# Optimization experiments

Hardware: AMD Instinct MI355X
Metric: run time of the kernel (lower is better)

## Reference

```python
import jax, jax.numpy as jnp
import numpy as np

IN_F = 1024
HID_F = 4096
OUT_F = 1024
B = 64
D = 768
SPARSE_RATIO = 0.1


def setup_inputs() -> dict:
    key = jax.random.key(0)
    k_x, k_w1, k_w2, k_b, k_m = jax.random.split(key, 5)
    # x: [batch, tokens(d), in_features(s)]
    x = jax.random.normal(k_x, (B, D, IN_F), dtype=jnp.float32)
    # scale weights like typical init so GELU inputs stay in a sane range
    fc1_w = jax.random.normal(k_w1, (HID_F, IN_F), dtype=jnp.float32) * (1.0 / np.sqrt(IN_F))
    fc2_w = jax.random.normal(k_w2, (OUT_F, HID_F), dtype=jnp.float32) * (1.0 / np.sqrt(HID_F))
    fc2_b = jax.random.normal(k_b, (OUT_F,), dtype=jnp.float32) * 0.02
    sparse_mask = (jax.random.uniform(k_m, (IN_F, OUT_F)) < SPARSE_RATIO).astype(jnp.float32)
    return {"x": x, "fc1_w": fc1_w, "fc2_w": fc2_w, "fc2_b": fc2_b, "sparse_mask": sparse_mask}


def reference(x, fc1_w, fc2_w, fc2_b, sparse_mask):
    # attn_s[s,t] = sum_d fc1_w[d,s] * fc2_w[t,d] + fc2_b[t]   -> [in, out]
    attn = (jnp.einsum('ds,td->st', fc1_w, fc2_w) + fc2_b) * sparse_mask
    # dropout with p=0.0 is the identity
    out = jnp.einsum('bds,st->bdt', x, attn)  # [B, D, out]
    # torch nn.GELU default is the exact (erf) variant
    return jax.nn.gelu(out, approximate=False)
```

## Files before the change

kernel.cpp:

```cpp
#include <hip/hip_runtime.h>
#include <hip/hip_bf16.h>
#include <math.h>

typedef __attribute__((ext_vector_type(8))) short  short8;
typedef __attribute__((ext_vector_type(4))) float  floatx4;
typedef __attribute__((ext_vector_type(4))) int    i32x4;

__device__ __forceinline__ ushort f2bf(float f) {
    __hip_bfloat16 hb = __float2bfloat16(f);
    return *(ushort*)&hb;
}
__device__ __forceinline__ short8 pack8(float4 a, float4 b) {
    union { short8 v; ushort u[8]; } r;
    r.u[0] = f2bf(a.x); r.u[1] = f2bf(a.y); r.u[2] = f2bf(a.z); r.u[3] = f2bf(a.w);
    r.u[4] = f2bf(b.x); r.u[5] = f2bf(b.y); r.u[6] = f2bf(b.z); r.u[7] = f2bf(b.w);
    return r.v;
}

typedef __attribute__((address_space(1))) const void* gas1_t;
typedef __attribute__((address_space(3))) void*       las3_t;
__device__ __forceinline__ void gload16(const void* g, void* l) {
    __builtin_amdgcn_global_load_lds((gas1_t)g, (las3_t)l, 16, 0, 0);
}
__device__ __forceinline__ short8 ds_read16(uint off) {
    union { i32x4 i; short8 s; } u;
    asm volatile("ds_read_b128 %0, %1" : "=v"(u.i) : "v"(off));
    return u.s;
}

__global__ __launch_bounds__(256) void k_cvt(const float* __restrict__ in,
                                             ushort* __restrict__ out, int n8) {
    int i = blockIdx.x * 256 + threadIdx.x;
    if (i >= n8) return;
    const float4* p = reinterpret_cast<const float4*>(in) + (size_t)i * 2;
    float4 a = p[0], b = p[1];
    *reinterpret_cast<short8*>(out + (size_t)i * 8) = pack8(a, b);
}

__global__ __launch_bounds__(256) void k_transpose(const float* __restrict__ in,
                                                   ushort* __restrict__ out) {
    __shared__ float sm[64][65];
    const int tid = threadIdx.x;
    const int s0 = blockIdx.x * 64;
    const int d0 = blockIdx.y * 64;
#pragma unroll
    for (int i = 0; i < 4; ++i) {
        int lin = i * 256 + tid;
        int dr  = lin >> 4;
        int sc4 = lin & 15;
        float4 v = *reinterpret_cast<const float4*>(&in[(size_t)(d0 + dr) * 1024 + s0 + sc4 * 4]);
        sm[dr][sc4 * 4 + 0] = v.x; sm[dr][sc4 * 4 + 1] = v.y;
        sm[dr][sc4 * 4 + 2] = v.z; sm[dr][sc4 * 4 + 3] = v.w;
    }
    __syncthreads();
#pragma unroll
    for (int i = 0; i < 8; ++i) {
        int lin = i * 256 + tid;
        int dc2 = lin & 31;
        int sr  = lin >> 5;
        uint lo = (uint)f2bf(sm[dc2 * 2][sr]);
        uint hi = (uint)f2bf(sm[dc2 * 2 + 1][sr]);
        *reinterpret_cast<uint*>(&out[(size_t)(s0 + sr) * 4096 + d0 + dc2 * 2]) = lo | (hi << 16);
    }
}

template <int BM, int BN, int EPI, int SWZ>
__global__ __launch_bounds__(256) void k_gemm_b(const ushort* __restrict__ A,
                                                const ushort* __restrict__ B,
                                                const float* __restrict__ bias,
                                                const float* __restrict__ mask,
                                                void* __restrict__ Cout,
                                                int lda, int ldb, int ksteps) {
    __shared__ ushort As[BM * 32];
    __shared__ ushort Bs[BN * 32];
    const int tid  = threadIdx.x;
    const int wave = tid >> 6, lane = tid & 63;
    const int wm = wave >> 1, wn = wave & 1;
    const int quad = lane >> 4, m16 = lane & 15;

    if (EPI == 2) {
        const int sp = blockIdx.z;
        A += (size_t)sp * 1024;
        B += (size_t)sp * 1024;
        Cout = (void*)((float*)Cout + (size_t)sp * 1048576);
    }

    int bx = blockIdx.x, by = blockIdx.y;
    if (SWZ) {
        const int nx   = gridDim.x;
        const int nwg  = nx * gridDim.y;
        const int orig = by * nx + bx;
        const int cpx  = nwg >> 3;
        const int w    = (orig & 7) * cpx + (orig >> 3);
        bx = w % nx; by = w / nx;
    }
    const int n0 = bx * BN;
    const int m0 = by * BM;

    constexpr int AI = BM / 32;
    constexpr int BJ = BN / 32;
    floatx4 acc[AI][BJ];
    const floatx4 zero = {0.f, 0.f, 0.f, 0.f};
#pragma unroll
    for (int i = 0; i < AI; ++i)
#pragma unroll
        for (int j = 0; j < BJ; ++j) acc[i][j] = zero;

    const int gr = lane >> 2;
    const int gc = (lane & 3) * 8;

    for (int kt = 0; kt < ksteps; ++kt) {
        const int k0 = kt * 32;
        if (kt) __syncthreads();
#pragma unroll
        for (int t = 0; t < BM / 64; ++t) {
            const int r = wave * (BM / 4) + t * 16;
            gload16(&A[(size_t)(m0 + r + gr) * lda + k0 + gc], &As[r * 32]);
        }
#pragma unroll
        for (int t = 0; t < BN / 64; ++t) {
            const int r = wave * (BN / 4) + t * 16;
            gload16(&B[(size_t)(n0 + r + gr) * ldb + k0 + gc], &Bs[r * 32]);
        }
        __syncthreads();

        short8 aF[AI], bF[BJ];
#pragma unroll
        for (int i = 0; i < AI; ++i)
            aF[i] = *reinterpret_cast<const short8*>(&As[(wm * (BM / 2) + i * 16 + m16) * 32 + quad * 8]);
#pragma unroll
        for (int j = 0; j < BJ; ++j)
            bF[j] = *reinterpret_cast<const short8*>(&Bs[(wn * (BN / 2) + j * 16 + m16) * 32 + quad * 8]);
#pragma unroll
        for (int i = 0; i < AI; ++i)
#pragma unroll
            for (int j = 0; j < BJ; ++j)
                acc[i][j] = __builtin_amdgcn_mfma_f32_16x16x32_bf16(aF[i], bF[j], acc[i][j], 0, 0, 0);
    }

#pragma unroll
    for (int i = 0; i < AI; ++i) {
#pragma unroll
        for (int j = 0; j < BJ; ++j) {
            const int col = n0 + wn * (BN / 2) + j * 16 + m16;
            float bv = 0.f;
            if (EPI == 0) bv = bias[col];
#pragma unroll
            for (int rr = 0; rr < 4; ++rr) {
                const int row = m0 + wm * (BM / 2) + i * 16 + quad * 4 + rr;
                float v = acc[i][j][rr];
                if (EPI == 0) {
                    v = (v + bv) * mask[(size_t)row * 1024 + col];
                    ((ushort*)Cout)[(size_t)col * 1024 + row] = f2bf(v);
                } else {
                    ((float*)Cout)[(size_t)row * 1024 + col] = v;
                }
            }
        }
    }
}

__global__ __launch_bounds__(256) void k_attn_fin(const float* __restrict__ P,
                                                  const float* __restrict__ bias,
                                                  const float* __restrict__ mask,
                                                  ushort* __restrict__ attnT) {
    __shared__ float sm[64][65];
    const int tid = threadIdx.x;
    const int s0 = blockIdx.x * 64;
    const int t0 = blockIdx.y * 64;
#pragma unroll
    for (int i = 0; i < 4; ++i) {
        int lin = i * 256 + tid;
        int sr  = lin >> 4;
        int tc4 = lin & 15;
        const size_t off = (size_t)(s0 + sr) * 1024 + t0 + tc4 * 4;
        float4 acc4 = *reinterpret_cast<const float4*>(&P[off]);
#pragma unroll
        for (int sp = 1; sp < 4; ++sp) {
            float4 v = *reinterpret_cast<const float4*>(&P[(size_t)sp * 1048576 + off]);
            acc4.x += v.x; acc4.y += v.y; acc4.z += v.z; acc4.w += v.w;
        }
        float4 bv = *reinterpret_cast<const float4*>(&bias[t0 + tc4 * 4]);
        float4 mk = *reinterpret_cast<const float4*>(&mask[(size_t)(s0 + sr) * 1024 + t0 + tc4 * 4]);
        sm[sr][tc4 * 4 + 0] = (acc4.x + bv.x) * mk.x;
        sm[sr][tc4 * 4 + 1] = (acc4.y + bv.y) * mk.y;
        sm[sr][tc4 * 4 + 2] = (acc4.z + bv.z) * mk.z;
        sm[sr][tc4 * 4 + 3] = (acc4.w + bv.w) * mk.w;
    }
    __syncthreads();
#pragma unroll
    for (int i = 0; i < 8; ++i) {
        int lin = i * 256 + tid;
        int sc2 = lin & 31;
        int tr  = lin >> 5;
        uint lo = (uint)f2bf(sm[sc2 * 2][tr]);
        uint hi = (uint)f2bf(sm[sc2 * 2 + 1][tr]);
        *reinterpret_cast<uint*>(&attnT[(size_t)(t0 + tr) * 1024 + s0 + sc2 * 2]) = lo | (hi << 16);
    }
}

#define SB __builtin_amdgcn_sched_barrier(0)
#define BAR __builtin_amdgcn_s_barrier()
#define LGKM(n) asm volatile("s_waitcnt lgkmcnt(" #n ")")
#define VMC(n)  asm volatile("s_waitcnt vmcnt(" #n ")")

#define RD_A(dst_, base_, ks_, mh_)                                             \
  { _Pragma("unroll")                                                           \
    for (int i_ = 0; i_ < 4; ++i_)                                              \
      dst_[i_] = ds_read16((base_) + (uint)((ks_)*16384 + ((mh_)*4 + i_)*1024)); }
#define RD_B(dst_, base_, ks_)                                                  \
  { _Pragma("unroll")                                                           \
    for (int j_ = 0; j_ < 4; ++j_)                                              \
      dst_[j_] = ds_read16((base_) + (uint)((ks_)*16384 + j_*1024)); }
#define MFMA16(aS_, bS_, MH_)                                                   \
  { __builtin_amdgcn_s_setprio(1);                                              \
    _Pragma("unroll")                                                           \
    for (int i_ = 0; i_ < 4; ++i_) {                                            \
      _Pragma("unroll")                                                         \
      for (int j_ = 0; j_ < 4; ++j_)                                            \
        acc[(MH_)*4 + i_][j_] = __builtin_amdgcn_mfma_f32_16x16x32_bf16(        \
            aS_[i_], bS_[j_], acc[(MH_)*4 + i_][j_], 0, 0, 0);                  \
    }                                                                           \
    __builtin_amdgcn_s_setprio(0); SB; }

#define BODY1(T_, bA_, bB_)                                                     \
  stage_ht(4*(T_) + 7); RD_A(a1, bA_, 0, 1);                                    \
  SB; BAR; SB; LGKM(4); SB; MFMA16(a0, b0, 0)
#define BODY2(T_, bA_, bB_)                                                     \
  stage_ht(4*(T_) + 8); RD_A(a2, bA_, 1, 0); RD_B(b1, bB_, 1);                  \
  SB; BAR; SB; LGKM(8); SB; MFMA16(a1, b0, 1)
#define BODY3(T_, bA_, bB_)                                                     \
  stage_ht(4*(T_) + 9); RD_A(a3, bA_, 1, 1);                                    \
  SB; BAR; SB; LGKM(4); SB; MFMA16(a2, b1, 0)
#define BODY4(T_, nA_, nB_, G_)                                                 \
  stage_ht(4*(T_) + 10); SB; VMC(G_); SB; BAR; SB;                              \
  RD_A(a0, nA_, 0, 0); RD_B(b0, nB_, 0);                                        \
  SB; LGKM(8); SB; MFMA16(a3, b1, 1)
#define BODY4F()                                                                \
  SB; BAR; SB; LGKM(0); SB; MFMA16(a3, b1, 1)

__global__ __launch_bounds__(512) void k_gemm8(const ushort* __restrict__ A,
                                               const ushort* __restrict__ B,
                                               float* __restrict__ C) {
    constexpr int NT = 16;
    __shared__ __align__(16) ushort lds[65536];

    const int tid  = threadIdx.x;
    const int wave = tid >> 6, lane = tid & 63;
    const int wm = wave >> 2, wn = wave & 3;
    const int quad = lane >> 4, m16 = lane & 15;

    const int orig = blockIdx.y * 4 + blockIdx.x;
    const int wsz  = (orig & 7) * 96 + (orig >> 3);
    const int n0 = (wsz & 3) * 256;
    const int m0 = (wsz >> 2) * 256;

    const uint lds0 = (uint)(size_t)(las3_t)(void*)lds;
    const uint xorM = (uint)((m16 & 6) << 3);
    const uint baseA = lds0 + ((((uint)(wm * 128 + m16)) * 64u + (uint)quad * 16u) ^ xorM);
    const uint baseB = lds0 + 32768u + ((((uint)(wn * 64 + m16)) * 64u + (uint)quad * 16u) ^ xorM);

    const int srow   = lane >> 2;
    const int schunk = (((lane & 3) ^ ((lane >> 3) & 3)) << 3);

    auto stage_ht = [&](int g) {
        if (g >= 4 * NT) return;
        const int tg = g >> 2, ig = g & 3;
        const int mat = ig & 1, ks = ig >> 1;
        const int kc  = tg * 64 + ks * 32 + schunk;
        const uint dst0 = (uint)(((tg & 1) << 16) | (mat << 15) | (ks << 14));
        const ushort* src = mat ? B : A;
        const int r0 = (mat ? n0 : m0) + srow;
#pragma unroll
        for (int e = 0; e < 2; ++e) {
            const int s = e * 8 + wave;
            gload16(&src[(size_t)(r0 + s * 16) * 1024 + kc],
                    (void*)((char*)lds + dst0 + (uint)(s << 10)));
        }
    };

    floatx4 acc[8][4];
    const floatx4 zf = {0.f, 0.f, 0.f, 0.f};
#pragma unroll
    for (int i = 0; i < 8; ++i)
#pragma unroll
        for (int j = 0; j < 4; ++j) acc[i][j] = zf;
    short8 a0[4], a1[4], a2[4], a3[4], b0[4], b1[4];

#pragma unroll
    for (int g = 0; g < 7; ++g) stage_ht(g);
    SB; VMC(6); SB; BAR; SB;
    RD_A(a0, baseA, 0, 0);
    RD_B(b0, baseB, 0);

    for (int tp = 0; tp < 7; ++tp) {
        const int t0 = 2 * tp, t1 = 2 * tp + 1;
        const uint cA = baseA, cB = baseB;
        const uint dA = baseA + 65536u, dB = baseB + 65536u;
        BODY1(t0, cA, cB); BODY2(t0, cA, cB); BODY3(t0, cA, cB);
        BODY4(t0, dA, dB, 6);
        BODY1(t1, dA, dB); BODY2(t1, dA, dB); BODY3(t1, dA, dB);
        BODY4(t1, cA, cB, 6);
    }
    {
        const uint cA = baseA, cB = baseB;
        const uint dA = baseA + 65536u, dB = baseB + 65536u;
        BODY1(14, cA, cB); BODY2(14, cA, cB); BODY3(14, cA, cB);
        BODY4(14, dA, dB, 0);
        BODY1(15, dA, dB); BODY2(15, dA, dB); BODY3(15, dA, dB);
        BODY4F();
    }

#pragma unroll
    for (int mf = 0; mf < 8; ++mf) {
#pragma unroll
        for (int nf = 0; nf < 4; ++nf) {
            const int col = n0 + wn * 64 + nf * 16 + m16;
#pragma unroll
            for (int rr = 0; rr < 4; ++rr) {
                const int row = m0 + wm * 128 + mf * 16 + quad * 4 + rr;
                const float v = acc[mf][nf][rr];
                C[(size_t)row * 1024 + col] = 0.5f * v * (1.0f + erff(v * 0.70710678118654752f));
            }
        }
    }
}

__global__ __launch_bounds__(256) void k_gemm_f32a(const float* __restrict__ Af,
                                                   const ushort* __restrict__ B,
                                                   float* __restrict__ Cout,
                                                   int lda, int ldb, int ksteps) {
    __shared__ ushort As[128 * 32];
    __shared__ ushort Bs[128 * 32];
    const int tid  = threadIdx.x;
    const int wave = tid >> 6, lane = tid & 63;
    const int wm = wave >> 1, wn = wave & 1;
    const int quad = lane >> 4, m16 = lane & 15;
    const int n0 = blockIdx.x * 128;
    const int m0 = blockIdx.y * 128;

    floatx4 acc[4][4];
    const floatx4 zero = {0.f, 0.f, 0.f, 0.f};
#pragma unroll
    for (int i = 0; i < 4; ++i)
#pragma unroll
        for (int j = 0; j < 4; ++j) acc[i][j] = zero;

    const int s_r = tid >> 2;
    const int s_c = tid & 3;
    const int gr = lane >> 2;
    const int gc = (lane & 3) * 8;

    for (int kt = 0; kt < ksteps; ++kt) {
        const int k0 = kt * 32;
        const float* r0 = &Af[(size_t)(m0 + s_r) * lda + k0 + s_c * 8];
        const float* r1 = &Af[(size_t)(m0 + 64 + s_r) * lda + k0 + s_c * 8];
        short8 a0 = pack8(*reinterpret_cast<const float4*>(r0), *reinterpret_cast<const float4*>(r0 + 4));
        short8 a1 = pack8(*reinterpret_cast<const float4*>(r1), *reinterpret_cast<const float4*>(r1 + 4));
        __syncthreads();
        *reinterpret_cast<short8*>(&As[(s_r)      * 32 + s_c * 8]) = a0;
        *reinterpret_cast<short8*>(&As[(64 + s_r) * 32 + s_c * 8]) = a1;
#pragma unroll
        for (int t = 0; t < 2; ++t) {
            const int r = wave * 32 + t * 16;
            gload16(&B[(size_t)(n0 + r + gr) * ldb + k0 + gc], &Bs[r * 32]);
        }
        __syncthreads();

        short8 aF[4], bF[4];
#pragma unroll
        for (int i = 0; i < 4; ++i)
            aF[i] = *reinterpret_cast<const short8*>(&As[(wm * 64 + i * 16 + m16) * 32 + quad * 8]);
#pragma unroll
        for (int j = 0; j < 4; ++j)
            bF[j] = *reinterpret_cast<const short8*>(&Bs[(wn * 64 + j * 16 + m16) * 32 + quad * 8]);
#pragma unroll
        for (int i = 0; i < 4; ++i)
#pragma unroll
            for (int j = 0; j < 4; ++j)
                acc[i][j] = __builtin_amdgcn_mfma_f32_16x16x32_bf16(aF[i], bF[j], acc[i][j], 0, 0, 0);
    }

#pragma unroll
    for (int i = 0; i < 4; ++i)
#pragma unroll
        for (int j = 0; j < 4; ++j) {
            const int col = n0 + wn * 64 + j * 16 + m16;
#pragma unroll
            for (int rr = 0; rr < 4; ++rr) {
                const int row = m0 + wm * 64 + i * 16 + quad * 4 + rr;
                float v = acc[i][j][rr];
                Cout[(size_t)row * 1024 + col] = 0.5f * v * (1.0f + erff(v * 0.70710678118654752f));
            }
        }
}

extern "C" void kernel_launch(void* const* d_in, const int* in_sizes, int n_in,
                              void* d_out, int out_size, void* d_ws, size_t ws_size,
                              hipStream_t stream) {
    const float* x    = (const float*)d_in[0];
    const float* fc1w = (const float*)d_in[1];
    const float* fc2w = (const float*)d_in[2];
    const float* fc2b = (const float*)d_in[3];
    const float* mask = (const float*)d_in[4];

    char* ws = (char*)d_ws;
    ushort* fc1T  = (ushort*)ws;
    ushort* fc2wb = (ushort*)(ws + (8u  << 20));
    ushort* attnT = (ushort*)(ws + (16u << 20));
    float*  attnP = (float*)(ws + (18u << 20));
    ushort* xb    = (ushort*)(ws + (18u << 20));
    const size_t XB_BYTES = 50331648ull * 2;
    const bool has_xb = ws_size >= (size_t)(18u << 20) + XB_BYTES;
    const bool has_p  = ws_size >= (size_t)(34u << 20);

    k_transpose<<<dim3(16, 64), 256, 0, stream>>>(fc1w, fc1T);
    k_cvt<<<2048, 256, 0, stream>>>(fc2w, fc2wb, 524288);

    if (has_p) {
        k_gemm_b<64, 64, 2, 1><<<dim3(16, 16, 4), 256, 0, stream>>>(
            fc1T, fc2wb, nullptr, nullptr, attnP, 4096, 4096, 32);
        k_attn_fin<<<dim3(16, 16), 256, 0, stream>>>(attnP, fc2b, mask, attnT);
    } else {
        k_gemm_b<64, 64, 0, 1><<<dim3(16, 16), 256, 0, stream>>>(
            fc1T, fc2wb, fc2b, mask, attnT, 4096, 4096, 128);
    }

    if (has_xb) {
        k_cvt<<<24576, 256, 0, stream>>>(x, xb, 6291456);
        k_gemm8<<<dim3(4, 192), 512, 0, stream>>>(xb, attnT, (float*)d_out);
    } else {
        k_gemm_f32a<<<dim3(8, 384), 256, 0, stream>>>(x, attnT, (float*)d_out, 1024, 1024, 32);
    }
}
```

Before: 553.3 us.

## Replace 256x256 eight-wave GEMM with 128x128 four-wave double-buffered kernel

Replaces the main x·attn GEMM, which used 256x256 tiles, 512 threads and a hand-interleaved 4-stage body, with a 128x128 tile kernel using 256 threads, launch bounds for 2 blocks per CU, a 64-wide K step, an XOR-swizzled LDS layout and a simple two-buffer stage/read/MFMA loop. The aim is higher occupancy and simpler scheduling, with two workgroups per CU hiding latency instead of the fine-grained software pipeline. In exchange, operand reuse per tile drops, which doubles global/L2 traffic for A and B, and the overlap inside each workgroup is coarser.

```diff
diff --git a/kernel.cpp b/kernel.cpp
--- a/kernel.cpp
+++ b/kernel.cpp
@@ -27,6 +27,11 @@
     asm volatile("ds_read_b128 %0, %1" : "=v"(u.i) : "v"(off));
     return u.s;
 }
+
+#define SB __builtin_amdgcn_sched_barrier(0)
+#define BAR __builtin_amdgcn_s_barrier()
+#define LGKM0 asm volatile("s_waitcnt lgkmcnt(0)")
+#define VMC(n)  asm volatile("s_waitcnt vmcnt(" #n ")")
 
 __global__ __launch_bounds__(256) void k_cvt(const float* __restrict__ in,
                                              ushort* __restrict__ out, int n8) {
@@ -199,131 +204,106 @@
     }
 }
 
-#define SB __builtin_amdgcn_sched_barrier(0)
-#define BAR __builtin_amdgcn_s_barrier()
-#define LGKM(n) asm volatile("s_waitcnt lgkmcnt(" #n ")")
-#define VMC(n)  asm volatile("s_waitcnt vmcnt(" #n ")")
-
-#define RD_A(dst_, base_, ks_, mh_)                                             \
-  { _Pragma("unroll")                                                           \
-    for (int i_ = 0; i_ < 4; ++i_)                                              \
-      dst_[i_] = ds_read16((base_) + (uint)((ks_)*16384 + ((mh_)*4 + i_)*1024)); }
-#define RD_B(dst_, base_, ks_)                                                  \
-  { _Pragma("unroll")                                                           \
-    for (int j_ = 0; j_ < 4; ++j_)                                              \
-      dst_[j_] = ds_read16((base_) + (uint)((ks_)*16384 + j_*1024)); }
-#define MFMA16(aS_, bS_, MH_)                                                   \
-  { __builtin_amdgcn_s_setprio(1);                                              \
-    _Pragma("unroll")                                                           \
-    for (int i_ = 0; i_ < 4; ++i_) {                                            \
-      _Pragma("unroll")                                                         \
-      for (int j_ = 0; j_ < 4; ++j_)                                            \
-        acc[(MH_)*4 + i_][j_] = __builtin_amdgcn_mfma_f32_16x16x32_bf16(        \
-            aS_[i_], bS_[j_], acc[(MH_)*4 + i_][j_], 0, 0, 0);                  \
-    }                                                                           \
-    __builtin_amdgcn_s_setprio(0); SB; }
-
-#define BODY1(T_, bA_, bB_)                                                     \
-  stage_ht(4*(T_) + 7); RD_A(a1, bA_, 0, 1);                                    \
-  SB; BAR; SB; LGKM(4); SB; MFMA16(a0, b0, 0)
-#define BODY2(T_, bA_, bB_)                                                     \
-  stage_ht(4*(T_) + 8); RD_A(a2, bA_, 1, 0); RD_B(b1, bB_, 1);                  \
-  SB; BAR; SB; LGKM(8); SB; MFMA16(a1, b0, 1)
-#define BODY3(T_, bA_, bB_)                                                     \
-  stage_ht(4*(T_) + 9); RD_A(a3, bA_, 1, 1);                                    \
-  SB; BAR; SB; LGKM(4); SB; MFMA16(a2, b1, 0)
-#define BODY4(T_, nA_, nB_, G_)                                                 \
-  stage_ht(4*(T_) + 10); SB; VMC(G_); SB; BAR; SB;                              \
-  RD_A(a0, nA_, 0, 0); RD_B(b0, nB_, 0);                                        \
-  SB; LGKM(8); SB; MFMA16(a3, b1, 1)
-#define BODY4F()                                                                \
-  SB; BAR; SB; LGKM(0); SB; MFMA16(a3, b1, 1)
-
-__global__ __launch_bounds__(512) void k_gemm8(const ushort* __restrict__ A,
-                                               const ushort* __restrict__ B,
-                                               float* __restrict__ C) {
-    constexpr int NT = 16;
-    __shared__ __align__(16) ushort lds[65536];
-
+__global__ __launch_bounds__(256, 2) void k_gemm2(const ushort* __restrict__ A,
+                                                  const ushort* __restrict__ B,
+                                                  float* __restrict__ C) {
+    __shared__ __align__(16) ushort lds[32768];
     const int tid  = threadIdx.x;
     const int wave = tid >> 6, lane = tid & 63;
-    const int wm = wave >> 2, wn = wave & 3;
+    const int wm = wave >> 1, wn = wave & 1;
     const int quad = lane >> 4, m16 = lane & 15;
 
-    const int orig = blockIdx.y * 4 + blockIdx.x;
-    const int wsz  = (orig & 7) * 96 + (orig >> 3);
-    const int n0 = (wsz & 3) * 256;
-    const int m0 = (wsz >> 2) * 256;
+    const int orig = blockIdx.y * 8 + blockIdx.x;
+    const int wsz  = (orig & 7) * 384 + (orig >> 3);
+    const int n0 = (wsz & 7) * 128;
+    const int m0 = (wsz >> 3) * 128;
 
     const uint lds0 = (uint)(size_t)(las3_t)(void*)lds;
-    const uint xorM = (uint)((m16 & 6) << 3);
-    const uint baseA = lds0 + ((((uint)(wm * 128 + m16)) * 64u + (uint)quad * 16u) ^ xorM);
-    const uint baseB = lds0 + 32768u + ((((uint)(wn * 64 + m16)) * 64u + (uint)quad * 16u) ^ xorM);
-
-    const int srow   = lane >> 2;
-    const int schunk = (((lane & 3) ^ ((lane >> 3) & 3)) << 3);
-
-    auto stage_ht = [&](int g) {
-        if (g >= 4 * NT) return;
-        const int tg = g >> 2, ig = g & 3;
-        const int mat = ig & 1, ks = ig >> 1;
-        const int kc  = tg * 64 + ks * 32 + schunk;
-        const uint dst0 = (uint)(((tg & 1) << 16) | (mat << 15) | (ks << 14));
-        const ushort* src = mat ? B : A;
-        const int r0 = (mat ? n0 : m0) + srow;
-#pragma unroll
-        for (int e = 0; e < 2; ++e) {
-            const int s = e * 8 + wave;
-            gload16(&src[(size_t)(r0 + s * 16) * 1024 + kc],
-                    (void*)((char*)lds + dst0 + (uint)(s << 10)));
-        }
+    const uint cs0 = (uint)(((0 + quad) ^ (m16 & 7)) << 4);
+    const uint cs1 = (uint)(((4 + quad) ^ (m16 & 7)) << 4);
+    const uint ldsA = lds0 + (uint)((wm * 64 + m16) * 128);
+    const uint ldsB = lds0 + 16384u + (uint)((wn * 64 + m16) * 128);
+
+    const int srow = lane >> 3;
+    const int cswz = (lane & 7) ^ srow;
+    const ushort* pA = A + (size_t)(m0 + wave * 32 + srow) * 1024 + cswz * 8;
+    const ushort* pB = B + (size_t)(n0 + wave * 32 + srow) * 1024 + cswz * 8;
+
+    auto stage = [&](int T) {
+        const uint bo = (uint)(T & 1) << 15;
+        const size_t colT = (size_t)T * 64;
+        char* dA = (char*)lds + bo + wave * 4096;
+        char* dB = (char*)lds + bo + 16384 + wave * 4096;
+#pragma unroll
+        for (int t = 0; t < 4; ++t)
+            gload16(pA + colT + (size_t)t * 8192, dA + t * 1024);
+#pragma unroll
+        for (int t = 0; t < 4; ++t)
+            gload16(pB + colT + (size_t)t * 8192, dB + t * 1024);
     };
 
-    floatx4 acc[8][4];
+    floatx4 acc[4][4];
     const floatx4 zf = {0.f, 0.f, 0.f, 0.f};
 #pragma unroll
-    for (int i = 0; i < 8; ++i)
+    for (int i = 0; i < 4; ++i)
 #pragma unroll
         for (int j = 0; j < 4; ++j) acc[i][j] = zf;
-    short8 a0[4], a1[4], a2[4], a3[4], b0[4], b1[4];
-
-#pragma unroll
-    for (int g = 0; g < 7; ++g) stage_ht(g);
-    SB; VMC(6); SB; BAR; SB;
-    RD_A(a0, baseA, 0, 0);
-    RD_B(b0, baseB, 0);
-
-    for (int tp = 0; tp < 7; ++tp) {
-        const int t0 = 2 * tp, t1 = 2 * tp + 1;
-        const uint cA = baseA, cB = baseB;
-        const uint dA = baseA + 65536u, dB = baseB + 65536u;
-        BODY1(t0, cA, cB); BODY2(t0, cA, cB); BODY3(t0, cA, cB);
-        BODY4(t0, dA, dB, 6);
-        BODY1(t1, dA, dB); BODY2(t1, dA, dB); BODY3(t1, dA, dB);
-        BODY4(t1, cA, cB, 6);
-    }
-    {
-        const uint cA = baseA, cB = baseB;
-        const uint dA = baseA + 65536u, dB = baseB + 65536u;
-        BODY1(14, cA, cB); BODY2(14, cA, cB); BODY3(14, cA, cB);
-        BODY4(14, dA, dB, 0);
-        BODY1(15, dA, dB); BODY2(15, dA, dB); BODY3(15, dA, dB);
-        BODY4F();
-    }
-
-#pragma unroll
-    for (int mf = 0; mf < 8; ++mf) {
-#pragma unroll
-        for (int nf = 0; nf < 4; ++nf) {
-            const int col = n0 + wn * 64 + nf * 16 + m16;
+
+    stage(0); stage(1);
+
+    short8 aF[2][4], bF[2][4];
+#define READS(bo_)                                                              \
+    { _Pragma("unroll")                                                         \
+      for (int i_ = 0; i_ < 4; ++i_) {                                          \
+        aF[0][i_] = ds_read16(ldsA + (bo_) + i_ * 2048 + cs0);                  \
+        aF[1][i_] = ds_read16(ldsA + (bo_) + i_ * 2048 + cs1);                  \
+      }                                                                         \
+      _Pragma("unroll")                                                         \
+      for (int j_ = 0; j_ < 4; ++j_) {                                          \
+        bF[0][j_] = ds_read16(ldsB + (bo_) + j_ * 2048 + cs0);                  \
+        bF[1][j_] = ds_read16(ldsB + (bo_) + j_ * 2048 + cs1);                  \
+      } }
+#define MFMA32                                                                  \
+    { __builtin_amdgcn_s_setprio(1);                                            \
+      _Pragma("unroll")                                                         \
+      for (int ks_ = 0; ks_ < 2; ++ks_)                                         \
+        _Pragma("unroll")                                                       \
+        for (int i_ = 0; i_ < 4; ++i_)                                          \
+          _Pragma("unroll")                                                     \
+          for (int j_ = 0; j_ < 4; ++j_)                                        \
+            acc[i_][j_] = __builtin_amdgcn_mfma_f32_16x16x32_bf16(              \
+                aF[ks_][i_], bF[ks_][j_], acc[i_][j_], 0, 0, 0);                \
+      __builtin_amdgcn_s_setprio(0); }
+
+    for (int T = 0; T < 15; ++T) {
+        VMC(8); SB; BAR; SB;
+        const uint bo = (uint)(T & 1) << 15;
+        READS(bo);
+        LGKM0; SB; BAR; SB;
+        if (T < 14) stage(T + 2);
+        SB;
+        MFMA32; SB;
+    }
+    VMC(0); SB; BAR; SB;
+    READS(32768u);
+    LGKM0; SB;
+    MFMA32;
+
+#pragma unroll
+    for (int i = 0; i < 4; ++i) {
+#pragma unroll
+        for (int j = 0; j < 4; ++j) {
+            const int col = n0 + wn * 64 + j * 16 + m16;
 #pragma unroll
             for (int rr = 0; rr < 4; ++rr) {
-                const int row = m0 + wm * 128 + mf * 16 + quad * 4 + rr;
-                const float v = acc[mf][nf][rr];
+                const int row = m0 + wm * 64 + i * 16 + quad * 4 + rr;
+                const float v = acc[i][j][rr];
                 C[(size_t)row * 1024 + col] = 0.5f * v * (1.0f + erff(v * 0.70710678118654752f));
             }
         }
     }
+#undef READS
+#undef MFMA32
 }
 
 __global__ __launch_bounds__(256) void k_gemm_f32a(const float* __restrict__ Af,
@@ -428,7 +408,7 @@
 
     if (has_xb) {
         k_cvt<<<24576, 256, 0, stream>>>(x, xb, 6291456);
-        k_gemm8<<<dim3(4, 192), 512, 0, stream>>>(xb, attnT, (float*)d_out);
+        k_gemm2<<<dim3(8, 384), 256, 0, stream>>>(xb, attnT, (float*)d_out);
     } else {
         k_gemm_f32a<<<dim3(8, 384), 256, 0, stream>>>(x, attnT, (float*)d_out, 1024, 1024, 32);
     }
```

Result: faster. 519.0 us (-6.2%).
